# Kernel optimization log

Measured on AMD Instinct MI355X. Metric: run time of the kernel, lower is better.

Reference implementation:

```python
import jax, jax.numpy as jnp
import numpy as np

BN_EPS = 1e-5   # BatchNorm2d eval-mode with default running stats (mean=0, var=1)
EPS = 1e-6      # PDNM self.eps


def _lin_idx(in_size, out_size, align):
    if align and out_size > 1:
        src = jnp.arange(out_size, dtype=jnp.float32) * ((in_size - 1) / (out_size - 1))
    else:
        src = jnp.clip((jnp.arange(out_size, dtype=jnp.float32) + 0.5) * (in_size / out_size) - 0.5,
                       0.0, in_size - 1)
    lo = jnp.floor(src).astype(jnp.int32)
    hi = jnp.minimum(lo + 1, in_size - 1)
    return lo, hi, src - lo


def resize_bilinear(x, oh, ow, align):
    # x: [n,c,h,w] -> [n,c,oh,ow], matches F.interpolate(mode='bilinear', align_corners=align)
    lo, hi, f = _lin_idx(x.shape[2], oh, align)
    x = x[:, :, lo, :] * (1.0 - f)[None, None, :, None] + x[:, :, hi, :] * f[None, None, :, None]
    lo, hi, f = _lin_idx(x.shape[3], ow, align)
    x = x[:, :, :, lo] * (1.0 - f) + x[:, :, :, hi] * f
    return x


def avg_pool(x, k):
    n, c, h, w = x.shape
    return x.reshape(n, c, h // k, k, w // k, k).mean(axis=(3, 5))


def max_pool2(x):
    n, c, h, w = x.shape
    return x.reshape(n, c, h // 2, 2, w // 2, 2).max(axis=(3, 5))


def conv1x1(x, w, b=None):
    y = jnp.einsum('nchw,oc->nohw', x, w)
    return y if b is None else y + b[None, :, None, None]


def pyramid_pool(x, pw, gamma, beta, ow, ob):
    # pw: [4, cc/4, cc]; gamma/beta: [4, cc/4]; ow: [cc, 2cc]; ob: [cc]
    H, W = x.shape[2], x.shape[3]
    outs = [x]
    for i, ps in enumerate((8, 4, 2, 1)):
        k = H // ps
        p = avg_pool(x, k)                                  # [n, cc, ps, ps]
        p = jnp.einsum('nchw,oc->nohw', p, pw[i])           # 1x1 conv, no bias
        p = p / np.sqrt(1.0 + BN_EPS) * gamma[i][None, :, None, None] + beta[i][None, :, None, None]
        p = jax.nn.relu(p)
        outs.append(resize_bilinear(p, H, W, False))        # F.upsample align_corners=False
    return conv1x1(jnp.concatenate(outs, axis=1), ow, ob)


def reference(x, depth_map, down_w, theta_w, theta_b, phi_w, phi_b, g_w, g_b, z_w, z_b,
              ppg_pw, ppg_gamma, ppg_beta, ppg_ow, ppg_ob,
              ppt_pw, ppt_gamma, ppt_beta, ppt_ow, ppt_ob,
              ppp_pw, ppp_gamma, ppp_beta, ppp_ow, ppp_ob):
    n, c, h, w = x.shape
    cc = c // 2
    # depthwise stride-4 conv (weight init 1/16 == 4x4 average, but learnable)
    x_down = jnp.einsum('nchawb,cab->nchw', x.reshape(n, c, h // 4, 4, w // 4, 4), down_w)
    g = max_pool2(conv1x1(x_down, g_w, g_b))                # [n, cc, h/8, w/8]
    g = pyramid_pool(g, ppg_pw, ppg_gamma, ppg_beta, ppg_ow, ppg_ob)
    g = g.reshape(n, cc, -1).transpose(0, 2, 1)             # [n, hw/64, cc]
    theta = pyramid_pool(conv1x1(x_down, theta_w, theta_b),
                         ppt_pw, ppt_gamma, ppt_beta, ppt_ow, ppt_ob)
    theta = theta.reshape(n, cc, -1).transpose(0, 2, 1)     # [n, hw/16, cc]
    phi = pyramid_pool(max_pool2(conv1x1(x_down, phi_w, phi_b)),
                       ppp_pw, ppp_gamma, ppp_beta, ppp_ow, ppp_ob)
    phi = phi.reshape(n, cc, -1)                            # [n, cc, hw/64]
    Ra = jax.nn.softmax(jnp.einsum('nqc,ncv->nqv', theta, phi), axis=2)
    d1 = resize_bilinear(depth_map, h // 4, w // 4, True).reshape(n, -1, 1)   # [n, hw/16, 1]
    d2 = resize_bilinear(depth_map, h // 8, w // 8, True).reshape(n, 1, -1)   # [n, 1, hw/64]
    Rd = jax.nn.softmax(jnp.minimum(d1 / (d2 + EPS), d2 / (d1 + EPS)), axis=2)
    S = jax.nn.softmax(Ra * Rd, axis=2)
    y = jnp.einsum('nqv,nvc->nqc', S, g).transpose(0, 2, 1).reshape(n, cc, h // 4, w // 4)
    return x + resize_bilinear(conv1x1(y, z_w, z_b), h, w, True)


def setup_inputs():
    key = jax.random.key(0)
    ks = iter(jax.random.split(key, 32))
    n, c, h, w = 4, 128, 256, 256
    cc = c // 2
    def W(shape, s=0.05):
        return jax.random.normal(next(ks), shape, jnp.float32) * s
    inp = {
        'x': W((n, c, h, w), 1.0),
        'depth_map': jax.random.uniform(next(ks), (n, 1, h, w), jnp.float32, 0.1, 10.0),
        'down_w': jnp.full((c, 4, 4), 1.0 / 16, jnp.float32),
        'theta_w': W((cc, c)), 'theta_b': jnp.zeros((cc,), jnp.float32),
        'phi_w': W((cc, c)), 'phi_b': jnp.zeros((cc,), jnp.float32),
        'g_w': W((cc, c)), 'g_b': jnp.zeros((cc,), jnp.float32),
        'z_w': W((c, cc)), 'z_b': jnp.zeros((c,), jnp.float32),
    }
    for p in ('ppg', 'ppt', 'ppp'):
        inp[p + '_pw'] = W((4, cc // 4, cc))
        inp[p + '_gamma'] = jnp.ones((4, cc // 4), jnp.float32)
        inp[p + '_beta'] = jnp.zeros((4, cc // 4), jnp.float32)
        inp[p + '_ow'] = W((cc, 2 * cc))
        inp[p + '_ob'] = jnp.zeros((cc,), jnp.float32)
    return inp
```

## Files before the change

kernel.cpp:

```cpp
#include <hip/hip_runtime.h>
#include <hip/hip_bf16.h>


typedef __bf16 bf16x8 __attribute__((ext_vector_type(8)));
typedef float f32x4 __attribute__((ext_vector_type(4)));

__device__ __forceinline__ ushort f2bf(float f) {
  uint b = __float_as_uint(f);
  uint r = (b + 0x7FFFu + ((b >> 16) & 1u)) >> 16;
  return (ushort)r;
}
__device__ __forceinline__ float red16max(float v) {
  v = fmaxf(v, __shfl_xor(v, 1, 64));
  v = fmaxf(v, __shfl_xor(v, 2, 64));
  v = fmaxf(v, __shfl_xor(v, 4, 64));
  v = fmaxf(v, __shfl_xor(v, 8, 64));
  return v;
}
__device__ __forceinline__ float red16sum(float v) {
  v += __shfl_xor(v, 1, 64);
  v += __shfl_xor(v, 2, 64);
  v += __shfl_xor(v, 4, 64);
  v += __shfl_xor(v, 8, 64);
  return v;
}

__global__ __launch_bounds__(256) void k_down(const float* __restrict__ x,
                                              const float* __restrict__ dw,
                                              float* __restrict__ xd) {
  const int n = blockIdx.z, c = blockIdx.y;
  const int p = blockIdx.x * 256 + threadIdx.x;
  const int i = p >> 6, j = p & 63;
  const float* xp = x + (((size_t)(n * 128 + c) * 256) + i * 4) * 256 + j * 4;
  const float* wp = dw + c * 16;
  float acc = 0.f;
#pragma unroll
  for (int a = 0; a < 4; ++a) {
    float4 v = *(const float4*)(xp + a * 256);
    acc += v.x * wp[a * 4 + 0] + v.y * wp[a * 4 + 1] + v.z * wp[a * 4 + 2] + v.w * wp[a * 4 + 3];
  }
  xd[(size_t)(n * 128 + c) * 4096 + p] = acc;
}

__global__ __launch_bounds__(256) void k_conv_cm4(const float* __restrict__ in,
                                                  const float* __restrict__ w,
                                                  const float* __restrict__ b,
                                                  float* __restrict__ out,
                                                  int Cin, int P, int O) {
  const int n = blockIdx.z, o4 = blockIdx.y * 4;
  const int p = blockIdx.x * 256 + threadIdx.x;
  const float* ip = in + (size_t)n * Cin * P + p;
  float a0 = b[o4], a1 = b[o4 + 1], a2 = b[o4 + 2], a3 = b[o4 + 3];
  const float* w0 = w + (size_t)o4 * Cin;
  const float* w1 = w0 + Cin;
  const float* w2 = w1 + Cin;
  const float* w3 = w2 + Cin;
  for (int c = 0; c < Cin; ++c) {
    const float v = ip[(size_t)c * P];
    a0 += v * w0[c]; a1 += v * w1[c]; a2 += v * w2[c]; a3 += v * w3[c];
  }
  size_t ob = ((size_t)n * O + o4) * P + p;
  out[ob] = a0; out[ob + P] = a1; out[ob + 2 * (size_t)P] = a2; out[ob + 3 * (size_t)P] = a3;
}

__global__ __launch_bounds__(256) void k_maxpool2(const float* __restrict__ in,
                                                  float* __restrict__ out,
                                                  int H, int W) {
  const int n = blockIdx.z, c = blockIdx.y;
  const int oh = H / 2, ow = W / 2;
  const int p = blockIdx.x * 256 + threadIdx.x;
  if (p >= oh * ow) return;
  const int i = p / ow, j = p % ow;
  const float* ip = in + ((size_t)(n * 64 + c) * H + 2 * i) * W + 2 * j;
  float m = fmaxf(fmaxf(ip[0], ip[1]), fmaxf(ip[W], ip[W + 1]));
  out[((size_t)(n * 64 + c) * oh + i) * ow + j] = m;
}

__global__ __launch_bounds__(256) void k_pool(const float* __restrict__ in,
                                              float* __restrict__ pooled, int H) {
  __shared__ float red[64][4];
  __shared__ float s8[64];
  const int blk = blockIdx.x;
  const int n = blk >> 6, c = blk & 63;
  const int t = threadIdx.x;
  const int cell = t & 63, part = t >> 6;
  const int gy = cell >> 3, gx = cell & 7;
  const int k = H >> 3;
  const int rpp = (k >> 2) ? (k >> 2) : 1;
  const float* base = in + (size_t)(n * 64 + c) * H * H;
  float s = 0.f;
  for (int r = 0; r < rpp; ++r) {
    const int y = gy * k + part * rpp + r;
    const float* rp = base + y * H + gx * k;
    for (int xx = 0; xx < k; xx += 4) {
      float4 v = *(const float4*)(rp + xx);
      s += v.x + v.y + v.z + v.w;
    }
  }
  red[cell][part] = s;
  __syncthreads();
  if (t < 64) s8[t] = red[t][0] + red[t][1] + red[t][2] + red[t][3];
  __syncthreads();
  float* pout = pooled + (size_t)(n * 64 + c) * 85;
  const float inv = 1.f / (float)(k * k);
  if (t < 64) {
    pout[t] = s8[t] * inv;
  } else if (t < 80) {
    const int i2 = t - 64, gy2 = i2 >> 2, gx2 = i2 & 3;
    float v = s8[(2 * gy2) * 8 + 2 * gx2] + s8[(2 * gy2) * 8 + 2 * gx2 + 1] +
              s8[(2 * gy2 + 1) * 8 + 2 * gx2] + s8[(2 * gy2 + 1) * 8 + 2 * gx2 + 1];
    pout[64 + i2] = v * inv * 0.25f;
  } else if (t < 84) {
    const int i1 = t - 80, gy1 = i1 >> 1, gx1 = i1 & 1;
    float v = 0.f;
    for (int yy = 0; yy < 4; ++yy)
      for (int xx = 0; xx < 4; ++xx) v += s8[(gy1 * 4 + yy) * 8 + gx1 * 4 + xx];
    pout[80 + i1] = v * inv * 0.0625f;
  } else if (t == 84) {
    float v = 0.f;
    for (int i = 0; i < 64; ++i) v += s8[i];
    pout[84] = v * inv * (1.f / 64.f);
  }
}

__global__ __launch_bounds__(256) void k_poolconv(const float* __restrict__ pooled,
                                                  const float* __restrict__ pw,
                                                  const float* __restrict__ gamma,
                                                  const float* __restrict__ beta,
                                                  float* __restrict__ qout) {
  const int n = blockIdx.x;
  const float bnscale = 0.9999950000374997f;
  for (int idx = threadIdx.x; idx < 85 * 16; idx += 256) {
    const int pos = idx >> 4, o = idx & 15;
    const int s = (pos < 64) ? 0 : (pos < 80) ? 1 : (pos < 84) ? 2 : 3;
    const float* pp = pooled + (size_t)n * 64 * 85 + pos;
    const float* wp = pw + (s * 16 + o) * 64;
    float acc = 0.f;
    for (int c = 0; c < 64; ++c) acc += pp[c * 85] * wp[c];
    acc = acc * bnscale * gamma[s * 16 + o] + beta[s * 16 + o];
    qout[((size_t)n * 85 + pos) * 16 + o] = fmaxf(acc, 0.f);
  }
}

__global__ __launch_bounds__(256) void k_ppfuse(const float* __restrict__ in,
                                                const float* __restrict__ q,
                                                const float* __restrict__ ow,
                                                const float* __restrict__ ob,
                                                ushort* __restrict__ out,
                                                int S, int lw, int pos_major) {
  __shared__ float bl[64][65];
  __shared__ float til[64][65];
  const int n = blockIdx.y;
  const int P = S * S;
  const int pixbase = blockIdx.x * 64;
  const int t = threadIdx.x;
  const int p = t & 63, sc = t >> 6;

  {
    const int pg = pixbase + p;
    const int y = pg >> lw, x = pg & (S - 1);
    const int ps = 8 >> sc;
    const int off = (sc == 0) ? 0 : (sc == 1) ? 64 : (sc == 2) ? 80 : 84;
    const float scale = (float)ps / (float)S;
    float syf = fminf(fmaxf((y + 0.5f) * scale - 0.5f, 0.f), (float)(ps - 1));
    float sxf = fminf(fmaxf((x + 0.5f) * scale - 0.5f, 0.f), (float)(ps - 1));
    const int ly = (int)syf, lx = (int)sxf;
    const int hy = min(ly + 1, ps - 1), hx = min(lx + 1, ps - 1);
    const float fy = syf - ly, fx = sxf - lx;
    const float w00 = (1.f - fy) * (1.f - fx), w01 = (1.f - fy) * fx;
    const float w10 = fy * (1.f - fx), w11 = fy * fx;
    const float* qn = q + (size_t)n * 85 * 16;
    const float4* r00 = (const float4*)(qn + (off + ly * ps + lx) * 16);
    const float4* r01 = (const float4*)(qn + (off + ly * ps + hx) * 16);
    const float4* r10 = (const float4*)(qn + (off + hy * ps + lx) * 16);
    const float4* r11 = (const float4*)(qn + (off + hy * ps + hx) * 16);
#pragma unroll
    for (int k = 0; k < 4; ++k) {
      float4 v00 = r00[k], v01 = r01[k], v10 = r10[k], v11 = r11[k];
      bl[p][sc * 16 + 4 * k + 0] = w00 * v00.x + w01 * v01.x + w10 * v10.x + w11 * v11.x;
      bl[p][sc * 16 + 4 * k + 1] = w00 * v00.y + w01 * v01.y + w10 * v10.y + w11 * v11.y;
      bl[p][sc * 16 + 4 * k + 2] = w00 * v00.z + w01 * v01.z + w10 * v10.z + w11 * v11.z;
      bl[p][sc * 16 + 4 * k + 3] = w00 * v00.w + w01 * v01.w + w10 * v10.w + w11 * v11.w;
    }
  }
  {
    const float* ip = in + (size_t)n * 64 * P + pixbase + p;
#pragma unroll
    for (int k = 0; k < 16; ++k) {
      const int c = sc + 4 * k;
      til[p][c] = ip[(size_t)c * P];
    }
  }
  __syncthreads();
  const int obase = sc * 16;
  float acc[16];
#pragma unroll
  for (int j = 0; j < 16; ++j) acc[j] = ob[obase + j];
  const float4* ow4 = (const float4*)ow;
#pragma unroll
  for (int c4 = 0; c4 < 16; ++c4) {
    const float4 tv = make_float4(til[p][4 * c4], til[p][4 * c4 + 1], til[p][4 * c4 + 2], til[p][4 * c4 + 3]);
    const float4 bv = make_float4(bl[p][4 * c4], bl[p][4 * c4 + 1], bl[p][4 * c4 + 2], bl[p][4 * c4 + 3]);
#pragma unroll
    for (int j = 0; j < 16; ++j) {
      const float4 wv = ow4[(obase + j) * 32 + c4];
      const float4 wb = ow4[(obase + j) * 32 + 16 + c4];
      acc[j] += tv.x * wv.x + tv.y * wv.y + tv.z * wv.z + tv.w * wv.w +
                bv.x * wb.x + bv.y * wb.y + bv.z * wb.z + bv.w * wb.w;
    }
  }
  if (pos_major) {
    __syncthreads();
#pragma unroll
    for (int j = 0; j < 16; ++j) til[p][obase + j] = acc[j];
    __syncthreads();
    const int p2 = t >> 2, c2 = (t & 3) * 16;
    uint pk[8];
#pragma unroll
    for (int i = 0; i < 8; ++i)
      pk[i] = (uint)f2bf(til[p2][c2 + 2 * i]) | ((uint)f2bf(til[p2][c2 + 2 * i + 1]) << 16);
    uint4* dst = (uint4*)(out + ((size_t)n * P + pixbase) * 64 + (size_t)t * 16);
    dst[0] = make_uint4(pk[0], pk[1], pk[2], pk[3]);
    dst[1] = make_uint4(pk[4], pk[5], pk[6], pk[7]);
  } else {
#pragma unroll
    for (int j = 0; j < 16; ++j)
      out[((size_t)n * 64 + obase + j) * P + pixbase + p] = f2bf(acc[j]);
  }
}

__global__ __launch_bounds__(256) void k_dresize(const float* __restrict__ depth,
                                                 float* __restrict__ d1,
                                                 float* __restrict__ d2) {
  const int n = blockIdx.y;
  const int bx = blockIdx.x;
  const float* dp = depth + (size_t)n * 65536;
  int i, j, idx;
  float scale;
  float* outp;
  if (bx < 16) {
    idx = bx * 256 + threadIdx.x;
    i = idx >> 6; j = idx & 63;
    scale = 255.f / 63.f;
    outp = d1 + (size_t)n * 4096;
  } else {
    idx = (bx - 16) * 256 + threadIdx.x;
    i = idx >> 5; j = idx & 31;
    scale = 255.f / 31.f;
    outp = d2 + (size_t)n * 1024;
  }
  const float sy = i * scale, sx = j * scale;
  const int ly = (int)sy, lx = (int)sx;
  const int hy = min(ly + 1, 255), hx = min(lx + 1, 255);
  const float fy = sy - ly, fx = sx - lx;
  const float v = (1.f - fy) * ((1.f - fx) * dp[ly * 256 + lx] + fx * dp[ly * 256 + hx]) +
                  fy * ((1.f - fx) * dp[hy * 256 + lx] + fx * dp[hy * 256 + hx]);
  outp[idx] = v;
}

__global__ __launch_bounds__(256) void k_attn(const ushort* __restrict__ thetaB,
                                              const ushort* __restrict__ phiB,
                                              const ushort* __restrict__ gB,
                                              const float* __restrict__ d1,
                                              const float* __restrict__ d2,
                                              float* __restrict__ yT) {
  __shared__ __align__(16) char smem[4 * 16 * 264 * 2];
  __shared__ float redl[4][16][4];
  __shared__ float spv[16];
  ushort* sbuf = (ushort*)smem;
  float* ypart = (float*)smem;

  const int n = blockIdx.y, q0 = blockIdx.x * 16;
  const int t = threadIdx.x, w = t >> 6, l = t & 63;
  const int lane16 = l & 15, quad = l >> 4;
  const int v0 = w * 256;

  f32x4 acc[16];
#pragma unroll
  for (int i = 0; i < 16; ++i) acc[i] = (f32x4){0.f, 0.f, 0.f, 0.f};
  const ushort* thA = thetaB + ((size_t)n * 4096 + q0 + lane16) * 64 + quad * 8;
  const ushort* phB = phiB + ((size_t)n * 1024 + v0 + lane16) * 64 + quad * 8;
#pragma unroll
  for (int ks = 0; ks < 2; ++ks) {
    bf16x8 av = *(const bf16x8*)(thA + ks * 32);
#pragma unroll
    for (int t16 = 0; t16 < 16; ++t16) {
      bf16x8 bv = *(const bf16x8*)(phB + t16 * 16 * 64 + ks * 32);
      acc[t16] = __builtin_amdgcn_mfma_f32_16x16x32_bf16(av, bv, acc[t16], 0, 0, 0);
    }
  }

  const float e6 = 1e-6f;
  float dq[4], iq[4];
  const float* d1p = d1 + (size_t)n * 4096 + q0 + quad * 4;
#pragma unroll
  for (int r = 0; r < 4; ++r) { dq[r] = d1p[r]; iq[r] = 1.f / (dq[r] + e6); }
  const float* d2p = d2 + (size_t)n * 1024 + v0 + lane16;

  float mx[4] = {-1e30f, -1e30f, -1e30f, -1e30f};
#pragma unroll
  for (int t16 = 0; t16 < 16; ++t16)
#pragma unroll
    for (int r = 0; r < 4; ++r) mx[r] = fmaxf(mx[r], acc[t16][r]);
#pragma unroll
  for (int r = 0; r < 4; ++r) mx[r] = red16max(mx[r]);
  if (lane16 == 0)
#pragma unroll
    for (int r = 0; r < 4; ++r) redl[w][quad * 4 + r][0] = mx[r];
  __syncthreads();
  float m[4];
#pragma unroll
  for (int r = 0; r < 4; ++r) {
    float v = redl[0][quad * 4 + r][0];
    v = fmaxf(v, redl[1][quad * 4 + r][0]);
    v = fmaxf(v, redl[2][quad * 4 + r][0]);
    m[r] = fmaxf(v, redl[3][quad * 4 + r][0]);
  }

  float se[4] = {0.f, 0.f, 0.f, 0.f}, sr[4] = {0.f, 0.f, 0.f, 0.f};
#pragma unroll
  for (int t16 = 0; t16 < 16; ++t16) {
    const float dd = d2p[t16 * 16];
    const float idd = 1.f / (dd + e6);
#pragma unroll
    for (int r = 0; r < 4; ++r) {
      const float rv = fminf(dq[r] * idd, dd * iq[r]);
      const float er = __expf(rv);
      const float ea = __expf(acc[t16][r] - m[r]);
      acc[t16][r] = ea * er;
      se[r] += ea; sr[r] += er;
    }
  }
#pragma unroll
  for (int r = 0; r < 4; ++r) { se[r] = red16sum(se[r]); sr[r] = red16sum(sr[r]); }
  if (lane16 == 0)
#pragma unroll
    for (int r = 0; r < 4; ++r) {
      redl[w][quad * 4 + r][1] = se[r];
      redl[w][quad * 4 + r][2] = sr[r];
    }
  __syncthreads();
  float U[4];
#pragma unroll
  for (int r = 0; r < 4; ++r) {
    const int row = quad * 4 + r;
    const float set = redl[0][row][1] + redl[1][row][1] + redl[2][row][1] + redl[3][row][1];
    const float srt = redl[0][row][2] + redl[1][row][2] + redl[2][row][2] + redl[3][row][2];
    U[r] = 1.f / (set * srt);
  }

  float sp[4] = {0.f, 0.f, 0.f, 0.f};
#pragma unroll
  for (int t16 = 0; t16 < 16; ++t16)
#pragma unroll
    for (int r = 0; r < 4; ++r) {
      const float s_ = __expf(U[r] * acc[t16][r]);
      acc[t16][r] = s_;
      sp[r] += s_;
    }
#pragma unroll
  for (int r = 0; r < 4; ++r) sp[r] = red16sum(sp[r]);
  if (lane16 == 0)
#pragma unroll
    for (int r = 0; r < 4; ++r) redl[w][quad * 4 + r][3] = sp[r];
  __syncthreads();
  if (w == 0 && lane16 == 0)
#pragma unroll
    for (int r = 0; r < 4; ++r) {
      const int row = quad * 4 + r;
      spv[row] = 1.f / (redl[0][row][3] + redl[1][row][3] + redl[2][row][3] + redl[3][row][3]);
    }

  ushort* srow = sbuf + w * (16 * 264);
#pragma unroll
  for (int t16 = 0; t16 < 16; ++t16)
#pragma unroll
    for (int r = 0; r < 4; ++r)
      srow[(quad * 4 + r) * 264 + t16 * 16 + lane16] = f2bf(acc[t16][r]);
  __syncthreads();

  f32x4 acc2[4];
#pragma unroll
  for (int i = 0; i < 4; ++i) acc2[i] = (f32x4){0.f, 0.f, 0.f, 0.f};
  const ushort* sA = sbuf + w * (16 * 264) + lane16 * 264 + quad * 8;
  const ushort* gq = gB + (size_t)n * 65536 + v0 + quad * 8;
#pragma unroll
  for (int kk = 0; kk < 8; ++kk) {
    bf16x8 av = *(const bf16x8*)(sA + kk * 32);
#pragma unroll
    for (int tn = 0; tn < 4; ++tn) {
      bf16x8 bv = *(const bf16x8*)(gq + (size_t)(tn * 16 + lane16) * 1024 + kk * 32);
      acc2[tn] = __builtin_amdgcn_mfma_f32_16x16x32_bf16(av, bv, acc2[tn], 0, 0, 0);
    }
  }
  __syncthreads();
  float* yp = ypart + w * (16 * 68);
#pragma unroll
  for (int tn = 0; tn < 4; ++tn)
#pragma unroll
    for (int r = 0; r < 4; ++r)
      yp[(quad * 4 + r) * 68 + tn * 16 + lane16] = acc2[tn][r];
  __syncthreads();
  const int row = t >> 4, c0 = (t & 15) * 4;
  float4 s0 = *(const float4*)(ypart + 0 * 1088 + row * 68 + c0);
  float4 s1 = *(const float4*)(ypart + 1 * 1088 + row * 68 + c0);
  float4 s2 = *(const float4*)(ypart + 2 * 1088 + row * 68 + c0);
  float4 s3 = *(const float4*)(ypart + 3 * 1088 + row * 68 + c0);
  const float isp = spv[row];
  float4 o;
  o.x = (s0.x + s1.x + s2.x + s3.x) * isp;
  o.y = (s0.y + s1.y + s2.y + s3.y) * isp;
  o.z = (s0.z + s1.z + s2.z + s3.z) * isp;
  o.w = (s0.w + s1.w + s2.w + s3.w) * isp;
  *(float4*)(yT + ((size_t)n * 4096 + q0 + row) * 64 + c0) = o;
}

__global__ __launch_bounds__(256) void k_zconv(const float* __restrict__ yT,
                                               const float* __restrict__ zw,
                                               const float* __restrict__ zb,
                                               float* __restrict__ z) {
  __shared__ float yt[64][65];
  const int n = blockIdx.y, p0 = blockIdx.x * 64;
  const int t = threadIdx.x;
  {
    const float4* src = (const float4*)(yT + ((size_t)n * 4096 + p0) * 64);
    const int p2 = t >> 2, c2 = (t & 3) * 16;
#pragma unroll
    for (int k = 0; k < 4; ++k) {
      float4 v = src[t * 4 + k];
      yt[p2][c2 + 4 * k + 0] = v.x; yt[p2][c2 + 4 * k + 1] = v.y;
      yt[p2][c2 + 4 * k + 2] = v.z; yt[p2][c2 + 4 * k + 3] = v.w;
    }
  }
  __syncthreads();
  const int p = t & 63, og = t >> 6;
  float acc[32];
#pragma unroll
  for (int j = 0; j < 32; ++j) acc[j] = zb[og * 32 + j];
  const float4* zw4 = (const float4*)zw;
#pragma unroll
  for (int c4 = 0; c4 < 16; ++c4) {
    const float4 yv = make_float4(yt[p][4 * c4], yt[p][4 * c4 + 1], yt[p][4 * c4 + 2], yt[p][4 * c4 + 3]);
#pragma unroll
    for (int j = 0; j < 32; ++j) {
      const float4 wv = zw4[(og * 32 + j) * 16 + c4];
      acc[j] += yv.x * wv.x + yv.y * wv.y + yv.z * wv.z + yv.w * wv.w;
    }
  }
  const size_t zb0 = ((size_t)n * 128 + og * 32) * 4096 + p0 + p;
#pragma unroll
  for (int j = 0; j < 32; ++j) z[zb0 + (size_t)j * 4096] = acc[j];
}

__global__ __launch_bounds__(256) void k_final(const float* __restrict__ x,
                                               const float* __restrict__ z,
                                               float* __restrict__ out) {
  const int n = blockIdx.z, c = blockIdx.y;
  const int Y = blockIdx.x * 4 + (threadIdx.x >> 6);
  const int X0 = (threadIdx.x & 63) * 4;
  const float s = 63.f / 255.f;
  const float sy = Y * s;
  const int ly = (int)sy;
  const int hy = min(ly + 1, 63);
  const float fy = sy - ly;
  const float* zp = z + (size_t)(n * 128 + c) * 4096;
  float4 o;
  float* po = &o.x;
#pragma unroll
  for (int k = 0; k < 4; ++k) {
    const float sx = (X0 + k) * s;
    const int lx = (int)sx;
    const int hx = min(lx + 1, 63);
    const float fx = sx - lx;
    po[k] = (1.f - fy) * ((1.f - fx) * zp[ly * 64 + lx] + fx * zp[ly * 64 + hx]) +
            fy * ((1.f - fx) * zp[hy * 64 + lx] + fx * zp[hy * 64 + hx]);
  }
  const size_t idx = ((size_t)(n * 128 + c) * 256 + Y) * 256 + X0;
  const float4 xv = *(const float4*)(x + idx);
  o.x += xv.x; o.y += xv.y; o.z += xv.z; o.w += xv.w;
  *(float4*)(out + idx) = o;
}

extern "C" void kernel_launch(void* const* d_in, const int* in_sizes, int n_in,
                              void* d_out, int out_size, void* d_ws, size_t ws_size,
                              hipStream_t stream) {
  const float* x       = (const float*)d_in[0];
  const float* depth   = (const float*)d_in[1];
  const float* down_w  = (const float*)d_in[2];
  const float* theta_w = (const float*)d_in[3];
  const float* theta_b = (const float*)d_in[4];
  const float* phi_w   = (const float*)d_in[5];
  const float* phi_b   = (const float*)d_in[6];
  const float* g_w     = (const float*)d_in[7];
  const float* g_b     = (const float*)d_in[8];
  const float* z_w     = (const float*)d_in[9];
  const float* z_b     = (const float*)d_in[10];
  const float* ppg_pw    = (const float*)d_in[11];
  const float* ppg_gamma = (const float*)d_in[12];
  const float* ppg_beta  = (const float*)d_in[13];
  const float* ppg_ow    = (const float*)d_in[14];
  const float* ppg_ob    = (const float*)d_in[15];
  const float* ppt_pw    = (const float*)d_in[16];
  const float* ppt_gamma = (const float*)d_in[17];
  const float* ppt_beta  = (const float*)d_in[18];
  const float* ppt_ow    = (const float*)d_in[19];
  const float* ppt_ob    = (const float*)d_in[20];
  const float* ppp_pw    = (const float*)d_in[21];
  const float* ppp_gamma = (const float*)d_in[22];
  const float* ppp_beta  = (const float*)d_in[23];
  const float* ppp_ow    = (const float*)d_in[24];
  const float* ppp_ob    = (const float*)d_in[25];

  float* ws = (float*)d_ws;
  float* xd       = ws;
  float* zbuf     = ws;
  float* t_in     = ws + 2097152;
  float* yT       = ws + 2097152;
  float* tmp      = ws + 3145728;
  float* phi_in   = ws + 4194304;
  float* g_in     = ws + 4456448;
  float* pooled_t = ws + 4718592;
  float* pooled_p = ws + 4740352;
  float* pooled_g = ws + 4762112;
  float* q_t      = ws + 4783872;
  float* q_p      = ws + 4789312;
  float* q_g      = ws + 4794752;
  ushort* thetaB  = (ushort*)(ws + 4800192);
  ushort* phiB    = (ushort*)(ws + 5324480);
  ushort* gB      = (ushort*)(ws + 5455552);
  float* d1       = ws + 5586624;
  float* d2       = ws + 5603008;

  dim3 b(256);
  k_down<<<dim3(16, 128, 4), b, 0, stream>>>(x, down_w, xd);
  k_conv_cm4<<<dim3(16, 16, 4), b, 0, stream>>>(xd, theta_w, theta_b, t_in, 128, 4096, 64);
  k_conv_cm4<<<dim3(16, 16, 4), b, 0, stream>>>(xd, phi_w, phi_b, tmp, 128, 4096, 64);
  k_maxpool2<<<dim3(4, 64, 4), b, 0, stream>>>(tmp, phi_in, 64, 64);
  k_conv_cm4<<<dim3(16, 16, 4), b, 0, stream>>>(xd, g_w, g_b, tmp, 128, 4096, 64);
  k_maxpool2<<<dim3(4, 64, 4), b, 0, stream>>>(tmp, g_in, 64, 64);
  k_dresize<<<dim3(20, 4), b, 0, stream>>>(depth, d1, d2);
  k_pool<<<dim3(256), b, 0, stream>>>(t_in, pooled_t, 64);
  k_pool<<<dim3(256), b, 0, stream>>>(phi_in, pooled_p, 32);
  k_pool<<<dim3(256), b, 0, stream>>>(g_in, pooled_g, 32);
  k_poolconv<<<dim3(4), b, 0, stream>>>(pooled_t, ppt_pw, ppt_gamma, ppt_beta, q_t);
  k_poolconv<<<dim3(4), b, 0, stream>>>(pooled_p, ppp_pw, ppp_gamma, ppp_beta, q_p);
  k_poolconv<<<dim3(4), b, 0, stream>>>(pooled_g, ppg_pw, ppg_gamma, ppg_beta, q_g);
  k_ppfuse<<<dim3(64, 4), b, 0, stream>>>(t_in, q_t, ppt_ow, ppt_ob, thetaB, 64, 6, 1);
  k_ppfuse<<<dim3(16, 4), b, 0, stream>>>(phi_in, q_p, ppp_ow, ppp_ob, phiB, 32, 5, 1);
  k_ppfuse<<<dim3(16, 4), b, 0, stream>>>(g_in, q_g, ppg_ow, ppg_ob, gB, 32, 5, 0);
  k_attn<<<dim3(256, 4), b, 0, stream>>>(thetaB, phiB, gB, d1, d2, yT);
  k_zconv<<<dim3(64, 4), b, 0, stream>>>(yT, z_w, z_b, zbuf);
  k_final<<<dim3(64, 128, 4), b, 0, stream>>>(x, zbuf, (float*)d_out);
}
```

Baseline: 580.4 us.

## Fuse projection convs into MFMA kernel and merge small pipeline stages

Replaces the three scalar 1x1 projection convs and two maxpool kernels with one bf16 MFMA kernel that computes theta/phi/g together and applies the 2x2 maxpool in registers. The bf16 weight packing is folded into an extra block of the downsample kernel. The pool, depth-resize, pool-conv and pyramid-fuse launches are merged across branches, and the z 1x1 conv is fused into the attention epilogue. The aim is to cut launch count and intermediate global traffic. The cost is bf16 rounding in the projection GEMM and more work in the attention kernel's tail.

```diff
diff --git a/kernel.cpp b/kernel.cpp
--- a/kernel.cpp
+++ b/kernel.cpp
@@ -27,9 +27,32 @@
 
 __global__ __launch_bounds__(256) void k_down(const float* __restrict__ x,
                                               const float* __restrict__ dw,
-                                              float* __restrict__ xd) {
-  const int n = blockIdx.z, c = blockIdx.y;
-  const int p = blockIdx.x * 256 + threadIdx.x;
+                                              float* __restrict__ xd,
+                                              const float* __restrict__ tw,
+                                              const float* __restrict__ tb,
+                                              const float* __restrict__ pw,
+                                              const float* __restrict__ pb,
+                                              const float* __restrict__ gw,
+                                              const float* __restrict__ gb,
+                                              ushort* __restrict__ Wb,
+                                              float* __restrict__ Bc) {
+  const int bid = blockIdx.x;
+  if (bid == 8192) {
+    for (int i = threadIdx.x; i < 192 * 128; i += 256) {
+      const int o = i >> 7, c = i & 127;
+      const float v = (o < 64) ? tw[o * 128 + c]
+                    : (o < 128) ? pw[(o - 64) * 128 + c]
+                                : gw[(o - 128) * 128 + c];
+      Wb[i] = f2bf(v);
+    }
+    if (threadIdx.x < 192) {
+      const int o = threadIdx.x;
+      Bc[o] = (o < 64) ? tb[o] : (o < 128) ? pb[o - 64] : gb[o - 128];
+    }
+    return;
+  }
+  const int n = bid >> 11, c = (bid >> 4) & 127;
+  const int p = (bid & 15) * 256 + threadIdx.x;
   const int i = p >> 6, j = p & 63;
   const float* xp = x + (((size_t)(n * 128 + c) * 256) + i * 4) * 256 + j * 4;
   const float* wp = dw + c * 16;
@@ -42,120 +65,225 @@
   xd[(size_t)(n * 128 + c) * 4096 + p] = acc;
 }
 
-__global__ __launch_bounds__(256) void k_conv_cm4(const float* __restrict__ in,
-                                                  const float* __restrict__ w,
-                                                  const float* __restrict__ b,
-                                                  float* __restrict__ out,
-                                                  int Cin, int P, int O) {
-  const int n = blockIdx.z, o4 = blockIdx.y * 4;
-  const int p = blockIdx.x * 256 + threadIdx.x;
-  const float* ip = in + (size_t)n * Cin * P + p;
-  float a0 = b[o4], a1 = b[o4 + 1], a2 = b[o4 + 2], a3 = b[o4 + 3];
-  const float* w0 = w + (size_t)o4 * Cin;
-  const float* w1 = w0 + Cin;
-  const float* w2 = w1 + Cin;
-  const float* w3 = w2 + Cin;
-  for (int c = 0; c < Cin; ++c) {
-    const float v = ip[(size_t)c * P];
-    a0 += v * w0[c]; a1 += v * w1[c]; a2 += v * w2[c]; a3 += v * w3[c];
-  }
-  size_t ob = ((size_t)n * O + o4) * P + p;
-  out[ob] = a0; out[ob + P] = a1; out[ob + 2 * (size_t)P] = a2; out[ob + 3 * (size_t)P] = a3;
-}
-
-__global__ __launch_bounds__(256) void k_maxpool2(const float* __restrict__ in,
-                                                  float* __restrict__ out,
-                                                  int H, int W) {
-  const int n = blockIdx.z, c = blockIdx.y;
-  const int oh = H / 2, ow = W / 2;
-  const int p = blockIdx.x * 256 + threadIdx.x;
-  if (p >= oh * ow) return;
-  const int i = p / ow, j = p % ow;
-  const float* ip = in + ((size_t)(n * 64 + c) * H + 2 * i) * W + 2 * j;
-  float m = fmaxf(fmaxf(ip[0], ip[1]), fmaxf(ip[W], ip[W + 1]));
-  out[((size_t)(n * 64 + c) * oh + i) * ow + j] = m;
-}
-
-__global__ __launch_bounds__(256) void k_pool(const float* __restrict__ in,
-                                              float* __restrict__ pooled, int H) {
+__global__ __launch_bounds__(256) void k_cfuse(const float* __restrict__ xd,
+                                               const ushort* __restrict__ Wb,
+                                               const float* __restrict__ Bc,
+                                               float* __restrict__ t_in,
+                                               float* __restrict__ phi_in,
+                                               float* __restrict__ g_in) {
+  __shared__ __align__(16) ushort xs[64 * 132];
+  const int bid = blockIdx.x;
+  const int n = bid >> 6, rp = (bid >> 1) & 31, jh = bid & 1;
+  const int t = threadIdx.x, w = t >> 6, l = t & 63;
+  {
+    const int rr = l >> 5, col = l & 31;
+    const int gpx = (2 * rp + rr) * 64 + jh * 32 + col;
+    const float* xsrc = xd + (size_t)n * 128 * 4096 + gpx;
+#pragma unroll
+    for (int k = 0; k < 32; ++k) {
+      const int c = w * 32 + k;
+      xs[l * 132 + c] = f2bf(xsrc[(size_t)c * 4096]);
+    }
+  }
+  __syncthreads();
+  const int lane16 = l & 15, quad = l >> 4;
+  f32x4 acc[3][4];
+#pragma unroll
+  for (int i = 0; i < 3; ++i)
+#pragma unroll
+    for (int nt = 0; nt < 4; ++nt) acc[i][nt] = (f32x4){0.f, 0.f, 0.f, 0.f};
+#pragma unroll
+  for (int ks = 0; ks < 4; ++ks) {
+    bf16x8 a[3];
+#pragma unroll
+    for (int i = 0; i < 3; ++i)
+      a[i] = *(const bf16x8*)(Wb + (size_t)((3 * w + i) * 16 + lane16) * 128 + ks * 32 + quad * 8);
+#pragma unroll
+    for (int nt = 0; nt < 4; ++nt) {
+      bf16x8 b = *(const bf16x8*)(xs + (nt * 16 + lane16) * 132 + ks * 32 + quad * 8);
+#pragma unroll
+      for (int i = 0; i < 3; ++i)
+        acc[i][nt] = __builtin_amdgcn_mfma_f32_16x16x32_bf16(a[i], b, acc[i][nt], 0, 0, 0);
+    }
+  }
+#pragma unroll
+  for (int i = 0; i < 3; ++i) {
+    const int tile = 3 * w + i;
+    const int ob = tile * 16 + quad * 4;
+    float bcv[4];
+#pragma unroll
+    for (int reg = 0; reg < 4; ++reg) bcv[reg] = Bc[ob + reg];
+    if (tile < 4) {
+#pragma unroll
+      for (int nt = 0; nt < 4; ++nt) {
+        const int px = nt * 16 + lane16, rr = px >> 5, cc = px & 31;
+        const size_t base = (size_t)(n * 64) * 4096 + (2 * rp + rr) * 64 + jh * 32 + cc;
+#pragma unroll
+        for (int reg = 0; reg < 4; ++reg)
+          t_in[base + (size_t)(ob + reg) * 4096] = acc[i][nt][reg] + bcv[reg];
+      }
+    } else {
+      const int o64 = ob - 64;
+      float* outp = (o64 < 64) ? phi_in : g_in;
+      const int oo = (o64 < 64) ? o64 : o64 - 64;
+#pragma unroll
+      for (int reg = 0; reg < 4; ++reg) {
+        float v0 = acc[i][0][reg] + bcv[reg];
+        float v1 = acc[i][1][reg] + bcv[reg];
+        float v2 = acc[i][2][reg] + bcv[reg];
+        float v3 = acc[i][3][reg] + bcv[reg];
+        float p0 = fmaxf(v0, v2);
+        float p1 = fmaxf(v1, v3);
+        p0 = fmaxf(p0, __shfl_xor(p0, 1, 64));
+        p1 = fmaxf(p1, __shfl_xor(p1, 1, 64));
+        if ((lane16 & 1) == 0) {
+          const int pc = lane16 >> 1;
+          const size_t d = ((size_t)(n * 64) + oo + reg) * 1024 + rp * 32 + jh * 16;
+          outp[d + pc] = p0;
+          outp[d + 8 + pc] = p1;
+        }
+      }
+    }
+  }
+}
+
+__global__ __launch_bounds__(256) void k_small(const float* __restrict__ t_in,
+                                               const float* __restrict__ phi_in,
+                                               const float* __restrict__ g_in,
+                                               float* __restrict__ pooled,
+                                               const float* __restrict__ depth,
+                                               float* __restrict__ d1,
+                                               float* __restrict__ d2) {
   __shared__ float red[64][4];
   __shared__ float s8[64];
-  const int blk = blockIdx.x;
-  const int n = blk >> 6, c = blk & 63;
+  const int bid = blockIdx.x;
   const int t = threadIdx.x;
-  const int cell = t & 63, part = t >> 6;
-  const int gy = cell >> 3, gx = cell & 7;
-  const int k = H >> 3;
-  const int rpp = (k >> 2) ? (k >> 2) : 1;
-  const float* base = in + (size_t)(n * 64 + c) * H * H;
-  float s = 0.f;
-  for (int r = 0; r < rpp; ++r) {
-    const int y = gy * k + part * rpp + r;
-    const float* rp = base + y * H + gx * k;
-    for (int xx = 0; xx < k; xx += 4) {
-      float4 v = *(const float4*)(rp + xx);
-      s += v.x + v.y + v.z + v.w;
-    }
-  }
-  red[cell][part] = s;
-  __syncthreads();
-  if (t < 64) s8[t] = red[t][0] + red[t][1] + red[t][2] + red[t][3];
-  __syncthreads();
-  float* pout = pooled + (size_t)(n * 64 + c) * 85;
-  const float inv = 1.f / (float)(k * k);
-  if (t < 64) {
-    pout[t] = s8[t] * inv;
-  } else if (t < 80) {
-    const int i2 = t - 64, gy2 = i2 >> 2, gx2 = i2 & 3;
-    float v = s8[(2 * gy2) * 8 + 2 * gx2] + s8[(2 * gy2) * 8 + 2 * gx2 + 1] +
-              s8[(2 * gy2 + 1) * 8 + 2 * gx2] + s8[(2 * gy2 + 1) * 8 + 2 * gx2 + 1];
-    pout[64 + i2] = v * inv * 0.25f;
-  } else if (t < 84) {
-    const int i1 = t - 80, gy1 = i1 >> 1, gx1 = i1 & 1;
-    float v = 0.f;
-    for (int yy = 0; yy < 4; ++yy)
-      for (int xx = 0; xx < 4; ++xx) v += s8[(gy1 * 4 + yy) * 8 + gx1 * 4 + xx];
-    pout[80 + i1] = v * inv * 0.0625f;
-  } else if (t == 84) {
-    float v = 0.f;
-    for (int i = 0; i < 64; ++i) v += s8[i];
-    pout[84] = v * inv * (1.f / 64.f);
-  }
-}
-
-__global__ __launch_bounds__(256) void k_poolconv(const float* __restrict__ pooled,
-                                                  const float* __restrict__ pw,
-                                                  const float* __restrict__ gamma,
-                                                  const float* __restrict__ beta,
-                                                  float* __restrict__ qout) {
-  const int n = blockIdx.x;
-  const float bnscale = 0.9999950000374997f;
-  for (int idx = threadIdx.x; idx < 85 * 16; idx += 256) {
-    const int pos = idx >> 4, o = idx & 15;
-    const int s = (pos < 64) ? 0 : (pos < 80) ? 1 : (pos < 84) ? 2 : 3;
-    const float* pp = pooled + (size_t)n * 64 * 85 + pos;
-    const float* wp = pw + (s * 16 + o) * 64;
-    float acc = 0.f;
-    for (int c = 0; c < 64; ++c) acc += pp[c * 85] * wp[c];
-    acc = acc * bnscale * gamma[s * 16 + o] + beta[s * 16 + o];
-    qout[((size_t)n * 85 + pos) * 16 + o] = fmaxf(acc, 0.f);
-  }
-}
-
-__global__ __launch_bounds__(256) void k_ppfuse(const float* __restrict__ in,
-                                                const float* __restrict__ q,
-                                                const float* __restrict__ ow,
-                                                const float* __restrict__ ob,
-                                                ushort* __restrict__ out,
-                                                int S, int lw, int pos_major) {
-  __shared__ float bl[64][65];
-  __shared__ float til[64][65];
-  const int n = blockIdx.y;
+  if (bid < 768) {
+    const int br = bid >> 8, blk = bid & 255;
+    const int n = blk >> 6, c = blk & 63;
+    const float* in = (br == 0) ? t_in : (br == 1) ? phi_in : g_in;
+    const int H = (br == 0) ? 64 : 32;
+    const int cell = t & 63, part = t >> 6;
+    const int gy = cell >> 3, gx = cell & 7;
+    const int k = H >> 3;
+    const int rpp = (k >> 2) ? (k >> 2) : 1;
+    const float* base = in + (size_t)(n * 64 + c) * H * H;
+    float s = 0.f;
+    for (int r = 0; r < rpp; ++r) {
+      const int y = gy * k + part * rpp + r;
+      const float* rpt = base + y * H + gx * k;
+      for (int xx = 0; xx < k; xx += 4) {
+        float4 v = *(const float4*)(rpt + xx);
+        s += v.x + v.y + v.z + v.w;
+      }
+    }
+    red[cell][part] = s;
+    __syncthreads();
+    if (t < 64) s8[t] = red[t][0] + red[t][1] + red[t][2] + red[t][3];
+    __syncthreads();
+    float* pout = pooled + ((size_t)(br * 4 + n) * 64 + c) * 85;
+    const float inv = 1.f / (float)(k * k);
+    if (t < 64) {
+      pout[t] = s8[t] * inv;
+    } else if (t < 80) {
+      const int i2 = t - 64, gy2 = i2 >> 2, gx2 = i2 & 3;
+      float v = s8[(2 * gy2) * 8 + 2 * gx2] + s8[(2 * gy2) * 8 + 2 * gx2 + 1] +
+                s8[(2 * gy2 + 1) * 8 + 2 * gx2] + s8[(2 * gy2 + 1) * 8 + 2 * gx2 + 1];
+      pout[64 + i2] = v * inv * 0.25f;
+    } else if (t < 84) {
+      const int i1 = t - 80, gy1 = i1 >> 1, gx1 = i1 & 1;
+      float v = 0.f;
+      for (int yy = 0; yy < 4; ++yy)
+        for (int xx = 0; xx < 4; ++xx) v += s8[(gy1 * 4 + yy) * 8 + gx1 * 4 + xx];
+      pout[80 + i1] = v * inv * 0.0625f;
+    } else if (t == 84) {
+      float v = 0.f;
+      for (int i = 0; i < 64; ++i) v += s8[i];
+      pout[84] = v * inv * (1.f / 64.f);
+    }
+  } else {
+    const int blk2 = bid - 768;
+    const int bx = blk2 >> 2, n = blk2 & 3;
+    const float* dp = depth + (size_t)n * 65536;
+    int i, j, idx;
+    float scale;
+    float* outp;
+    if (bx < 16) {
+      idx = bx * 256 + t;
+      i = idx >> 6; j = idx & 63;
+      scale = 255.f / 63.f;
+      outp = d1 + (size_t)n * 4096;
+    } else {
+      idx = (bx - 16) * 256 + t;
+      i = idx >> 5; j = idx & 31;
+      scale = 255.f / 31.f;
+      outp = d2 + (size_t)n * 1024;
+    }
+    const float sy = i * scale, sx = j * scale;
+    const int ly = (int)sy, lx = (int)sx;
+    const int hy = min(ly + 1, 255), hx = min(lx + 1, 255);
+    const float fy = sy - ly, fx = sx - lx;
+    const float v = (1.f - fy) * ((1.f - fx) * dp[ly * 256 + lx] + fx * dp[ly * 256 + hx]) +
+                    fy * ((1.f - fx) * dp[hy * 256 + lx] + fx * dp[hy * 256 + hx]);
+    outp[idx] = v;
+  }
+}
+
+__global__ __launch_bounds__(256) void k_ppfuse3(
+    const float* __restrict__ t_in, const float* __restrict__ phi_in,
+    const float* __restrict__ g_in, const float* __restrict__ pooled,
+    const float* __restrict__ tpw, const float* __restrict__ tga, const float* __restrict__ tbe,
+    const float* __restrict__ tow, const float* __restrict__ tob,
+    const float* __restrict__ ppw, const float* __restrict__ pga, const float* __restrict__ pbe,
+    const float* __restrict__ pow_, const float* __restrict__ pob,
+    const float* __restrict__ gpw, const float* __restrict__ gga, const float* __restrict__ gbe,
+    const float* __restrict__ gow, const float* __restrict__ gob,
+    ushort* __restrict__ thetaB, ushort* __restrict__ phiB, ushort* __restrict__ gB) {
+  __shared__ __align__(16) float sh[9680];
+  float* q_s = sh;
+  float* bl = sh + 1360;
+  float* til = sh + 5520;
+  float* pooled_s = sh + 1360;
+
+  const int bx = blockIdx.x, n = blockIdx.y;
+  const int t = threadIdx.x;
+  int br, tile;
+  if (bx < 64) { br = 0; tile = bx; }
+  else if (bx < 80) { br = 1; tile = bx - 64; }
+  else { br = 2; tile = bx - 80; }
+  const int S = (br == 0) ? 64 : 32;
+  const int lw = (br == 0) ? 6 : 5;
+  const int pm = (br == 2) ? 0 : 1;
+  const float* in = (br == 0) ? t_in : (br == 1) ? phi_in : g_in;
+  const float* pw = (br == 0) ? tpw : (br == 1) ? ppw : gpw;
+  const float* ga = (br == 0) ? tga : (br == 1) ? pga : gga;
+  const float* be = (br == 0) ? tbe : (br == 1) ? pbe : gbe;
+  const float* owp = (br == 0) ? tow : (br == 1) ? pow_ : gow;
+  const float* obp = (br == 0) ? tob : (br == 1) ? pob : gob;
+  ushort* out = (br == 0) ? thetaB : (br == 1) ? phiB : gB;
   const int P = S * S;
-  const int pixbase = blockIdx.x * 64;
-  const int t = threadIdx.x;
+  const int pixbase = tile * 64;
+
+  {
+    const float* pb_ = pooled + ((size_t)(br * 4 + n) * 64) * 85;
+    for (int i = t; i < 5440; i += 256) pooled_s[i] = pb_[i];
+  }
+  __syncthreads();
+  {
+    const float bnscale = 0.9999950000374997f;
+    for (int idx = t; idx < 85 * 16; idx += 256) {
+      const int pos = idx >> 4, o = idx & 15;
+      const int s = (pos < 64) ? 0 : (pos < 80) ? 1 : (pos < 84) ? 2 : 3;
+      const float* wp = pw + (s * 16 + o) * 64;
+      float acc = 0.f;
+      for (int c = 0; c < 64; ++c) acc += pooled_s[c * 85 + pos] * wp[c];
+      acc = acc * bnscale * ga[s * 16 + o] + be[s * 16 + o];
+      q_s[idx] = fmaxf(acc, 0.f);
+    }
+  }
+  __syncthreads();
+
   const int p = t & 63, sc = t >> 6;
-
   {
     const int pg = pixbase + p;
     const int y = pg >> lw, x = pg & (S - 1);
@@ -169,18 +297,17 @@
     const float fy = syf - ly, fx = sxf - lx;
     const float w00 = (1.f - fy) * (1.f - fx), w01 = (1.f - fy) * fx;
     const float w10 = fy * (1.f - fx), w11 = fy * fx;
-    const float* qn = q + (size_t)n * 85 * 16;
-    const float4* r00 = (const float4*)(qn + (off + ly * ps + lx) * 16);
-    const float4* r01 = (const float4*)(qn + (off + ly * ps + hx) * 16);
-    const float4* r10 = (const float4*)(qn + (off + hy * ps + lx) * 16);
-    const float4* r11 = (const float4*)(qn + (off + hy * ps + hx) * 16);
+    const float4* r00 = (const float4*)(q_s + (off + ly * ps + lx) * 16);
+    const float4* r01 = (const float4*)(q_s + (off + ly * ps + hx) * 16);
+    const float4* r10 = (const float4*)(q_s + (off + hy * ps + lx) * 16);
+    const float4* r11 = (const float4*)(q_s + (off + hy * ps + hx) * 16);
 #pragma unroll
     for (int k = 0; k < 4; ++k) {
       float4 v00 = r00[k], v01 = r01[k], v10 = r10[k], v11 = r11[k];
-      bl[p][sc * 16 + 4 * k + 0] = w00 * v00.x + w01 * v01.x + w10 * v10.x + w11 * v11.x;
-      bl[p][sc * 16 + 4 * k + 1] = w00 * v00.y + w01 * v01.y + w10 * v10.y + w11 * v11.y;
-      bl[p][sc * 16 + 4 * k + 2] = w00 * v00.z + w01 * v01.z + w10 * v10.z + w11 * v11.z;
-      bl[p][sc * 16 + 4 * k + 3] = w00 * v00.w + w01 * v01.w + w10 * v10.w + w11 * v11.w;
+      bl[p * 65 + sc * 16 + 4 * k + 0] = w00 * v00.x + w01 * v01.x + w10 * v10.x + w11 * v11.x;
+      bl[p * 65 + sc * 16 + 4 * k + 1] = w00 * v00.y + w01 * v01.y + w10 * v10.y + w11 * v11.y;
+      bl[p * 65 + sc * 16 + 4 * k + 2] = w00 * v00.z + w01 * v01.z + w10 * v10.z + w11 * v11.z;
+      bl[p * 65 + sc * 16 + 4 * k + 3] = w00 * v00.w + w01 * v01.w + w10 * v10.w + w11 * v11.w;
     }
   }
   {
@@ -188,19 +315,21 @@
 #pragma unroll
     for (int k = 0; k < 16; ++k) {
       const int c = sc + 4 * k;
-      til[p][c] = ip[(size_t)c * P];
+      til[p * 65 + c] = ip[(size_t)c * P];
     }
   }
   __syncthreads();
   const int obase = sc * 16;
   float acc[16];
 #pragma unroll
-  for (int j = 0; j < 16; ++j) acc[j] = ob[obase + j];
-  const float4* ow4 = (const float4*)ow;
+  for (int j = 0; j < 16; ++j) acc[j] = obp[obase + j];
+  const float4* ow4 = (const float4*)owp;
 #pragma unroll
   for (int c4 = 0; c4 < 16; ++c4) {
-    const float4 tv = make_float4(til[p][4 * c4], til[p][4 * c4 + 1], til[p][4 * c4 + 2], til[p][4 * c4 + 3]);
-    const float4 bv = make_float4(bl[p][4 * c4], bl[p][4 * c4 + 1], bl[p][4 * c4 + 2], bl[p][4 * c4 + 3]);
+    const float4 tv = make_float4(til[p * 65 + 4 * c4], til[p * 65 + 4 * c4 + 1],
+                                  til[p * 65 + 4 * c4 + 2], til[p * 65 + 4 * c4 + 3]);
+    const float4 bv = make_float4(bl[p * 65 + 4 * c4], bl[p * 65 + 4 * c4 + 1],
+                                  bl[p * 65 + 4 * c4 + 2], bl[p * 65 + 4 * c4 + 3]);
 #pragma unroll
     for (int j = 0; j < 16; ++j) {
       const float4 wv = ow4[(obase + j) * 32 + c4];
@@ -209,16 +338,16 @@
                 bv.x * wb.x + bv.y * wb.y + bv.z * wb.z + bv.w * wb.w;
     }
   }
-  if (pos_major) {
+  if (pm) {
     __syncthreads();
 #pragma unroll
-    for (int j = 0; j < 16; ++j) til[p][obase + j] = acc[j];
+    for (int j = 0; j < 16; ++j) til[p * 65 + obase + j] = acc[j];
     __syncthreads();
     const int p2 = t >> 2, c2 = (t & 3) * 16;
     uint pk[8];
 #pragma unroll
     for (int i = 0; i < 8; ++i)
-      pk[i] = (uint)f2bf(til[p2][c2 + 2 * i]) | ((uint)f2bf(til[p2][c2 + 2 * i + 1]) << 16);
+      pk[i] = (uint)f2bf(til[p2 * 65 + c2 + 2 * i]) | ((uint)f2bf(til[p2 * 65 + c2 + 2 * i + 1]) << 16);
     uint4* dst = (uint4*)(out + ((size_t)n * P + pixbase) * 64 + (size_t)t * 16);
     dst[0] = make_uint4(pk[0], pk[1], pk[2], pk[3]);
     dst[1] = make_uint4(pk[4], pk[5], pk[6], pk[7]);
@@ -227,35 +356,6 @@
     for (int j = 0; j < 16; ++j)
       out[((size_t)n * 64 + obase + j) * P + pixbase + p] = f2bf(acc[j]);
   }
-}
-
-__global__ __launch_bounds__(256) void k_dresize(const float* __restrict__ depth,
-                                                 float* __restrict__ d1,
-                                                 float* __restrict__ d2) {
-  const int n = blockIdx.y;
-  const int bx = blockIdx.x;
-  const float* dp = depth + (size_t)n * 65536;
-  int i, j, idx;
-  float scale;
-  float* outp;
-  if (bx < 16) {
-    idx = bx * 256 + threadIdx.x;
-    i = idx >> 6; j = idx & 63;
-    scale = 255.f / 63.f;
-    outp = d1 + (size_t)n * 4096;
-  } else {
-    idx = (bx - 16) * 256 + threadIdx.x;
-    i = idx >> 5; j = idx & 31;
-    scale = 255.f / 31.f;
-    outp = d2 + (size_t)n * 1024;
-  }
-  const float sy = i * scale, sx = j * scale;
-  const int ly = (int)sy, lx = (int)sx;
-  const int hy = min(ly + 1, 255), hx = min(lx + 1, 255);
-  const float fy = sy - ly, fx = sx - lx;
-  const float v = (1.f - fy) * ((1.f - fx) * dp[ly * 256 + lx] + fx * dp[ly * 256 + hx]) +
-                  fy * ((1.f - fx) * dp[hy * 256 + lx] + fx * dp[hy * 256 + hx]);
-  outp[idx] = v;
 }
 
 __global__ __launch_bounds__(256) void k_attn(const ushort* __restrict__ thetaB,
@@ -263,12 +363,15 @@
                                               const ushort* __restrict__ gB,
                                               const float* __restrict__ d1,
                                               const float* __restrict__ d2,
-                                              float* __restrict__ yT) {
+                                              const float* __restrict__ zw,
+                                              const float* __restrict__ zb,
+                                              float* __restrict__ z) {
   __shared__ __align__(16) char smem[4 * 16 * 264 * 2];
   __shared__ float redl[4][16][4];
   __shared__ float spv[16];
   ushort* sbuf = (ushort*)smem;
   float* ypart = (float*)smem;
+  float* ycomb = (float*)smem + 4352;
 
   const int n = blockIdx.y, q0 = blockIdx.x * 16;
   const int t = threadIdx.x, w = t >> 6, l = t & 63;
@@ -401,55 +504,40 @@
     for (int r = 0; r < 4; ++r)
       yp[(quad * 4 + r) * 68 + tn * 16 + lane16] = acc2[tn][r];
   __syncthreads();
-  const int row = t >> 4, c0 = (t & 15) * 4;
-  float4 s0 = *(const float4*)(ypart + 0 * 1088 + row * 68 + c0);
-  float4 s1 = *(const float4*)(ypart + 1 * 1088 + row * 68 + c0);
-  float4 s2 = *(const float4*)(ypart + 2 * 1088 + row * 68 + c0);
-  float4 s3 = *(const float4*)(ypart + 3 * 1088 + row * 68 + c0);
-  const float isp = spv[row];
-  float4 o;
-  o.x = (s0.x + s1.x + s2.x + s3.x) * isp;
-  o.y = (s0.y + s1.y + s2.y + s3.y) * isp;
-  o.z = (s0.z + s1.z + s2.z + s3.z) * isp;
-  o.w = (s0.w + s1.w + s2.w + s3.w) * isp;
-  *(float4*)(yT + ((size_t)n * 4096 + q0 + row) * 64 + c0) = o;
-}
-
-__global__ __launch_bounds__(256) void k_zconv(const float* __restrict__ yT,
-                                               const float* __restrict__ zw,
-                                               const float* __restrict__ zb,
-                                               float* __restrict__ z) {
-  __shared__ float yt[64][65];
-  const int n = blockIdx.y, p0 = blockIdx.x * 64;
-  const int t = threadIdx.x;
   {
-    const float4* src = (const float4*)(yT + ((size_t)n * 4096 + p0) * 64);
-    const int p2 = t >> 2, c2 = (t & 3) * 16;
-#pragma unroll
-    for (int k = 0; k < 4; ++k) {
-      float4 v = src[t * 4 + k];
-      yt[p2][c2 + 4 * k + 0] = v.x; yt[p2][c2 + 4 * k + 1] = v.y;
-      yt[p2][c2 + 4 * k + 2] = v.z; yt[p2][c2 + 4 * k + 3] = v.w;
-    }
-  }
-  __syncthreads();
-  const int p = t & 63, og = t >> 6;
-  float acc[32];
-#pragma unroll
-  for (int j = 0; j < 32; ++j) acc[j] = zb[og * 32 + j];
-  const float4* zw4 = (const float4*)zw;
-#pragma unroll
-  for (int c4 = 0; c4 < 16; ++c4) {
-    const float4 yv = make_float4(yt[p][4 * c4], yt[p][4 * c4 + 1], yt[p][4 * c4 + 2], yt[p][4 * c4 + 3]);
-#pragma unroll
-    for (int j = 0; j < 32; ++j) {
-      const float4 wv = zw4[(og * 32 + j) * 16 + c4];
-      acc[j] += yv.x * wv.x + yv.y * wv.y + yv.z * wv.z + yv.w * wv.w;
-    }
-  }
-  const size_t zb0 = ((size_t)n * 128 + og * 32) * 4096 + p0 + p;
-#pragma unroll
-  for (int j = 0; j < 32; ++j) z[zb0 + (size_t)j * 4096] = acc[j];
+    const int row = t >> 4, c0 = (t & 15) * 4;
+    float4 s0 = *(const float4*)(ypart + 0 * 1088 + row * 68 + c0);
+    float4 s1 = *(const float4*)(ypart + 1 * 1088 + row * 68 + c0);
+    float4 s2 = *(const float4*)(ypart + 2 * 1088 + row * 68 + c0);
+    float4 s3 = *(const float4*)(ypart + 3 * 1088 + row * 68 + c0);
+    const float isp = spv[row];
+    float4 o;
+    o.x = (s0.x + s1.x + s2.x + s3.x) * isp;
+    o.y = (s0.y + s1.y + s2.y + s3.y) * isp;
+    o.z = (s0.z + s1.z + s2.z + s3.z) * isp;
+    o.w = (s0.w + s1.w + s2.w + s3.w) * isp;
+    *(float4*)(ycomb + row * 68 + c0) = o;
+  }
+  __syncthreads();
+  {
+    const int px = t & 15, og = t >> 4;
+    float a8[8];
+#pragma unroll
+    for (int j = 0; j < 8; ++j) a8[j] = zb[og * 8 + j];
+    const float4* zw4 = (const float4*)zw;
+#pragma unroll
+    for (int c4 = 0; c4 < 16; ++c4) {
+      const float4 yv = *(const float4*)(ycomb + px * 68 + c4 * 4);
+#pragma unroll
+      for (int j = 0; j < 8; ++j) {
+        const float4 wv = zw4[(og * 8 + j) * 16 + c4];
+        a8[j] += yv.x * wv.x + yv.y * wv.y + yv.z * wv.z + yv.w * wv.w;
+      }
+    }
+    const size_t zb0 = ((size_t)n * 128 + og * 8) * 4096 + q0 + px;
+#pragma unroll
+    for (int j = 0; j < 8; ++j) z[zb0 + (size_t)j * 4096] = a8[j];
+  }
 }
 
 __global__ __launch_bounds__(256) void k_final(const float* __restrict__ x,
@@ -512,43 +600,30 @@
   const float* ppp_ob    = (const float*)d_in[25];
 
   float* ws = (float*)d_ws;
-  float* xd       = ws;
-  float* zbuf     = ws;
-  float* t_in     = ws + 2097152;
-  float* yT       = ws + 2097152;
-  float* tmp      = ws + 3145728;
-  float* phi_in   = ws + 4194304;
-  float* g_in     = ws + 4456448;
-  float* pooled_t = ws + 4718592;
-  float* pooled_p = ws + 4740352;
-  float* pooled_g = ws + 4762112;
-  float* q_t      = ws + 4783872;
-  float* q_p      = ws + 4789312;
-  float* q_g      = ws + 4794752;
-  ushort* thetaB  = (ushort*)(ws + 4800192);
-  ushort* phiB    = (ushort*)(ws + 5324480);
-  ushort* gB      = (ushort*)(ws + 5455552);
-  float* d1       = ws + 5586624;
-  float* d2       = ws + 5603008;
+  float* xd      = ws;
+  float* zbuf    = ws;
+  float* t_in    = ws + 2097152;
+  float* phi_in  = ws + 3145728;
+  float* g_in    = ws + 3407872;
+  float* pooled  = ws + 3670016;
+  float* d1      = ws + 3735296;
+  float* d2      = ws + 3751680;
+  ushort* thetaB = (ushort*)(ws + 3755776);
+  ushort* phiB   = (ushort*)(ws + 4280064);
+  ushort* gB     = (ushort*)(ws + 4411136);
+  ushort* Wb     = (ushort*)(ws + 4542208);
+  float* Bc      = ws + 4554496;
 
   dim3 b(256);
-  k_down<<<dim3(16, 128, 4), b, 0, stream>>>(x, down_w, xd);
-  k_conv_cm4<<<dim3(16, 16, 4), b, 0, stream>>>(xd, theta_w, theta_b, t_in, 128, 4096, 64);
-  k_conv_cm4<<<dim3(16, 16, 4), b, 0, stream>>>(xd, phi_w, phi_b, tmp, 128, 4096, 64);
-  k_maxpool2<<<dim3(4, 64, 4), b, 0, stream>>>(tmp, phi_in, 64, 64);
-  k_conv_cm4<<<dim3(16, 16, 4), b, 0, stream>>>(xd, g_w, g_b, tmp, 128, 4096, 64);
-  k_maxpool2<<<dim3(4, 64, 4), b, 0, stream>>>(tmp, g_in, 64, 64);
-  k_dresize<<<dim3(20, 4), b, 0, stream>>>(depth, d1, d2);
-  k_pool<<<dim3(256), b, 0, stream>>>(t_in, pooled_t, 64);
-  k_pool<<<dim3(256), b, 0, stream>>>(phi_in, pooled_p, 32);
-  k_pool<<<dim3(256), b, 0, stream>>>(g_in, pooled_g, 32);
-  k_poolconv<<<dim3(4), b, 0, stream>>>(pooled_t, ppt_pw, ppt_gamma, ppt_beta, q_t);
-  k_poolconv<<<dim3(4), b, 0, stream>>>(pooled_p, ppp_pw, ppp_gamma, ppp_beta, q_p);
-  k_poolconv<<<dim3(4), b, 0, stream>>>(pooled_g, ppg_pw, ppg_gamma, ppg_beta, q_g);
-  k_ppfuse<<<dim3(64, 4), b, 0, stream>>>(t_in, q_t, ppt_ow, ppt_ob, thetaB, 64, 6, 1);
-  k_ppfuse<<<dim3(16, 4), b, 0, stream>>>(phi_in, q_p, ppp_ow, ppp_ob, phiB, 32, 5, 1);
-  k_ppfuse<<<dim3(16, 4), b, 0, stream>>>(g_in, q_g, ppg_ow, ppg_ob, gB, 32, 5, 0);
-  k_attn<<<dim3(256, 4), b, 0, stream>>>(thetaB, phiB, gB, d1, d2, yT);
-  k_zconv<<<dim3(64, 4), b, 0, stream>>>(yT, z_w, z_b, zbuf);
+  k_down<<<dim3(8193), b, 0, stream>>>(x, down_w, xd, theta_w, theta_b, phi_w, phi_b,
+                                       g_w, g_b, Wb, Bc);
+  k_cfuse<<<dim3(256), b, 0, stream>>>(xd, Wb, Bc, t_in, phi_in, g_in);
+  k_small<<<dim3(848), b, 0, stream>>>(t_in, phi_in, g_in, pooled, depth, d1, d2);
+  k_ppfuse3<<<dim3(96, 4), b, 0, stream>>>(t_in, phi_in, g_in, pooled,
+                                           ppt_pw, ppt_gamma, ppt_beta, ppt_ow, ppt_ob,
+                                           ppp_pw, ppp_gamma, ppp_beta, ppp_ow, ppp_ob,
+                                           ppg_pw, ppg_gamma, ppg_beta, ppg_ow, ppg_ob,
+                                           thetaB, phiB, gB);
+  k_attn<<<dim3(256, 4), b, 0, stream>>>(thetaB, phiB, gB, d1, d2, z_w, z_b, zbuf);
   k_final<<<dim3(64, 128, 4), b, 0, stream>>>(x, zbuf, (float*)d_out);
 }
```

Result: faster. 471.0 us (-18.8%).
